# Kernel tuning notes

Hardware: AMD Instinct MI355X
Metric: run time of the kernel (lower is better)

## Reference

```python
import jax, jax.numpy as jnp
import numpy as np

N = 8192          # nodes per type (MiRNA, Disease, T)
E = 500000        # edges per relation
FEAT = 256
HID = 64
OUT = 128
ITEM = 8192
SIZE = 4096
LEFT = 0
# relation order: 0:MvsD(M->D) 1:DvsM(D->M) 2:MvsT(M->T) 3:TvsM(T->M) 4:TvsD(T->D) 5:DvsT(D->T)


def graph_conv(x, W, b, src, dst, n_src, n_dst):
    outdeg = jax.ops.segment_sum(jnp.ones(src.shape, x.dtype), src, num_segments=n_src)
    xs = (x * (jnp.maximum(outdeg, 1.0) ** -0.5)[:, None]) @ W
    agg = jax.ops.segment_sum(xs[src], dst, num_segments=n_dst)
    indeg = jax.ops.segment_sum(jnp.ones(dst.shape, x.dtype), dst, num_segments=n_dst)
    return agg * (jnp.maximum(indeg, 1.0) ** -0.5)[:, None] + b


def hetero_layer(hM, hD, hT, W, b, edges):
    srcs = [hM, hD, hM, hT, hT, hD]
    outs = [graph_conv(srcs[i], W[i], b[i], edges[i, 0], edges[i, 1], N, N) for i in range(6)]
    # aggregate='sum' per destination type
    newM = outs[1] + outs[3]
    newD = outs[0] + outs[4]
    newT = outs[2] + outs[5]
    return newM, newD, newT


def setup_inputs() -> dict:
    key = jax.random.key(0)
    ks = jax.random.split(key, 24)

    def glorot(k, shape):
        lim = np.sqrt(6.0 / (shape[-2] + shape[-1]))
        return jax.random.uniform(k, shape, jnp.float32, -lim, lim)

    inp = {
        'hM': jax.random.normal(ks[0], (N, FEAT), jnp.float32),
        'hD': jax.random.normal(ks[1], (N, FEAT), jnp.float32),
        'hT': jax.random.normal(ks[2], (N, FEAT), jnp.float32),
        'W1': glorot(ks[3], (6, FEAT, HID)), 'b1': jnp.zeros((6, HID), jnp.float32),
        'W2': glorot(ks[4], (6, HID, HID)), 'b2': jnp.zeros((6, HID), jnp.float32),
        'W3': glorot(ks[5], (6, HID, OUT)), 'b3': jnp.zeros((6, OUT), jnp.float32),
        'Adj': (jax.random.uniform(ks[6], (SIZE, ITEM)) < 0.05).astype(jnp.float32),
        'f1_w': glorot(ks[7], (ITEM + OUT, 256)), 'f1_b': jnp.zeros((256,), jnp.float32),
        'f2_w': glorot(ks[8], (256, 512)), 'f2_b': jnp.zeros((512,), jnp.float32),
        'f3_w': glorot(ks[9], (512, 1024)), 'f3_b': jnp.zeros((1024,), jnp.float32),
        'f4_w': glorot(ks[10], (1024, ITEM)), 'f4_b': jnp.zeros((ITEM,), jnp.float32),
        'edges': jax.random.randint(ks[11], (6, 2, E), 0, N, dtype=jnp.int32),
        'size': SIZE,
        'leftIndex': LEFT,
    }
    return inp


def reference(hM, hD, hT, W1, b1, W2, b2, W3, b3, Adj,
              f1_w, f1_b, f2_w, f2_b, f3_w, f3_b, f4_w, f4_b,
              edges, size, leftIndex):
    hM1, hD1, hT1 = hetero_layer(hM, hD, hT, W1, b1, edges)
    hM2, hD2, hT2 = hetero_layer(hM1, hD1, hT1, W2, b2, edges)
    hM3, hD3, hT3 = hetero_layer(hM2, hD2, hT2, W3, b3, edges)
    # torch.nn.functional.normalize(p=1, dim=1)
    mirna = hM3 / jnp.maximum(jnp.sum(jnp.abs(hM3), axis=1, keepdims=True), 1e-12)
    fake_embeding = mirna[leftIndex:leftIndex + size]
    M = jnp.concatenate([Adj, fake_embeding], axis=1)
    x = jax.nn.relu(M @ f1_w + f1_b)
    x = jax.nn.relu(x @ f2_w + f2_b)
    x = jax.nn.relu(x @ f3_w + f3_b)
    x = jax.nn.sigmoid(x @ f4_w + f4_b)
    return fake_embeding, x
```

## Files before the change

### kernel.cpp

```cpp
#include <hip/hip_runtime.h>
#include <hip/hip_bf16.h>
#include <cstdint>
#include <cstddef>
#include <type_traits>

#define NN 8192
#define NTYPE 6
#define BPT 32

typedef __attribute__((ext_vector_type(8))) short bf16x8;
typedef __attribute__((ext_vector_type(4))) float f32x4;
typedef __attribute__((ext_vector_type(4))) unsigned short u16x4;
typedef __attribute__((ext_vector_type(8))) unsigned short u16x8;

#define GLOAD16(g, l)                                                        \
  __builtin_amdgcn_global_load_lds(                                          \
      (const __attribute__((address_space(1))) void*)(g),                    \
      (__attribute__((address_space(3))) void*)(l), 16, 0, 0)

static __device__ __forceinline__ unsigned short f2bf(float f) {
  union { float f; unsigned u; } x; x.f = f;
  unsigned u = x.u + 0x7fffu + ((x.u >> 16) & 1u);
  return (unsigned short)(u >> 16);
}
static __device__ __forceinline__ float bf2f(unsigned short u) {
  union { unsigned u32; float f; } x; x.u32 = (unsigned)u << 16; return x.f;
}

__global__ __launch_bounds__(256) void hist_degree(
    const int* __restrict__ edges, int* __restrict__ partial, int E) {
  const int b = blockIdx.x, t = blockIdx.y, role = blockIdx.z;
  __shared__ int h[NN];
  for (int i = threadIdx.x; i < NN; i += 256) h[i] = 0;
  __syncthreads();
  const int* ids = edges + ((size_t)t * 2 + role) * E;
  int ch = (E + BPT - 1) / BPT;
  int beg = b * ch, end = (beg + ch < E) ? beg + ch : E;
  for (int i = beg + threadIdx.x; i < end; i += 256)
    atomicAdd(&h[__builtin_nontemporal_load(ids + i)], 1);
  __syncthreads();
  int* dst = partial + ((size_t)((role * NTYPE + t) * BPT + b)) * NN;
  for (int i = threadIdx.x; i < NN; i += 256) dst[i] = h[i];
}

__global__ __launch_bounds__(256) void reduce_deg(
    const int* __restrict__ partial, float* __restrict__ inv_out,
    float* __restrict__ inv_in, int* __restrict__ incnt) {
  int i = blockIdx.x * 256 + threadIdx.x;
  if (i >= NTYPE * NN) return;
  int t = i >> 13, n = i & (NN - 1);
  const int* ps = partial + ((size_t)(t * BPT)) * NN + n;
  const int* pd = partial + ((size_t)((NTYPE + t) * BPT)) * NN + n;
  int so = 0, sd = 0;
#pragma unroll 8
  for (int b = 0; b < BPT; ++b) { so += ps[(size_t)b * NN]; sd += pd[(size_t)b * NN]; }
  inv_out[i] = rsqrtf(fmaxf((float)so, 1.0f));
  inv_in[i]  = rsqrtf(fmaxf((float)sd, 1.0f));
  incnt[i]   = sd;
}

__global__ void scan_rows(const int* __restrict__ incnt, int* __restrict__ row_start) {
  int t = blockIdx.x;
  int i = threadIdx.x;
  const int* c = incnt + t * NN;
  int v[8], s = 0;
#pragma unroll
  for (int j = 0; j < 8; ++j) { v[j] = c[i * 8 + j]; s += v[j]; }
  __shared__ int p[1024];
  p[i] = s;
  __syncthreads();
  for (int d = 1; d < 1024; d <<= 1) {
    int x = (i >= d) ? p[i - d] : 0;
    __syncthreads();
    p[i] += x;
    __syncthreads();
  }
  int run = p[i] - s;
  int* rs = row_start + t * (NN + 1);
#pragma unroll
  for (int j = 0; j < 8; ++j) { rs[i * 8 + j] = run; run += v[j]; }
  if (i == 1023) rs[NN] = run;
}

__global__ __launch_bounds__(256) void slice_offsets(
    const int* __restrict__ partial, const int* __restrict__ row_start,
    int* __restrict__ soff) {
  int i = blockIdx.x * 256 + threadIdx.x;
  if (i >= NTYPE * NN) return;
  int t = i >> 13, d = i & (NN - 1);
  const int* pd = partial + ((size_t)((NTYPE + t) * BPT)) * NN + d;
  int run = row_start[t * (NN + 1) + d];
  int* o = soff + ((size_t)t * BPT) * NN + d;
#pragma unroll 8
  for (int s = 0; s < BPT; ++s) { o[(size_t)s * NN] = run; run += pd[(size_t)s * NN]; }
}

__global__ __launch_bounds__(256) void scatter_v2(
    const int* __restrict__ edges, const int* __restrict__ soff,
    int* __restrict__ csr, int E) {
  int t = blockIdx.x;
  if (t >= NTYPE) return;
  int s = blockIdx.y;
  __shared__ int cur[NN];
  const int* o = soff + ((size_t)(t * BPT + s)) * NN;
  for (int i = threadIdx.x; i < NN; i += 256) cur[i] = o[i];
  __syncthreads();
  int ch = (E + BPT - 1) / BPT;
  int beg = s * ch, end = (beg + ch < E) ? beg + ch : E;
  const int* eb = edges + (size_t)t * 2 * E;
  int* out = csr + (size_t)t * E;
  for (int i = beg + threadIdx.x; i < end; i += 256) {
    int src = __builtin_nontemporal_load(eb + i);
    int dst = __builtin_nontemporal_load(eb + E + i);
    int pos = atomicAdd(&cur[dst], 1);
    out[pos] = src;
  }
}

__global__ __launch_bounds__(256) void gemm64xs(
    const float* __restrict__ p0, const float* __restrict__ p1,
    const float* __restrict__ p2, int lda,
    const float* __restrict__ WL, const float* __restrict__ inv_out,
    unsigned short* __restrict__ xs6, int F, int H, int tpack) {
  const int t = (tpack >> (4 * blockIdx.z)) & 15;
  const int srcc[6] = {0, 1, 0, 2, 2, 1};
  const float* A = (srcc[t] == 0) ? p0 : (srcc[t] == 1) ? p1 : p2;
  const float* B = WL + (size_t)t * F * H;
  const float* rscale = inv_out + t * NN;
  unsigned short* out = xs6 + (size_t)t * NN * H;

  __shared__ float As[16][68];
  __shared__ float Bs[16][68];
  int tid = threadIdx.x;
  int n0 = blockIdx.x * 64, m0 = blockIdx.y * 64;
  int ar = tid >> 2, ac = (tid & 3) * 4;
  int br = tid >> 4, bc = (tid & 15) * 4;
  int tx = tid & 15, ty = tid >> 4;
  float acc[4][4] = {};
  for (int k0 = 0; k0 < F; k0 += 16) {
    float4 av = *(const float4*)(A + (size_t)(m0 + ar) * lda + k0 + ac);
    As[ac + 0][ar] = av.x; As[ac + 1][ar] = av.y;
    As[ac + 2][ar] = av.z; As[ac + 3][ar] = av.w;
    *(float4*)&Bs[br][bc] = *(const float4*)(B + (size_t)(k0 + br) * H + n0 + bc);
    __syncthreads();
#pragma unroll
    for (int kk = 0; kk < 16; ++kk) {
      float4 a = *(const float4*)&As[kk][ty * 4];
      float4 b = *(const float4*)&Bs[kk][tx * 4];
      float aa[4] = {a.x, a.y, a.z, a.w};
      float bb[4] = {b.x, b.y, b.z, b.w};
#pragma unroll
      for (int i = 0; i < 4; ++i)
#pragma unroll
        for (int j = 0; j < 4; ++j) acc[i][j] += aa[i] * bb[j];
    }
    __syncthreads();
  }
#pragma unroll
  for (int i = 0; i < 4; ++i) {
    int r = m0 + ty * 4 + i;
    float sc = rscale[r];
    union { unsigned short us[4]; short4 v; } pk;
#pragma unroll
    for (int j = 0; j < 4; ++j) pk.us[j] = f2bf(acc[i][j] * sc);
    *(short4*)&out[(size_t)r * H + n0 + tx * 4] = pk.v;
  }
}

template <int H>
__global__ __launch_bounds__(256) void aggregate3(
    const unsigned short* __restrict__ xs6, const int* __restrict__ csr,
    const int* __restrict__ row_start, const float* __restrict__ inv_in,
    const float* __restrict__ bL, float* __restrict__ feat_out, int E, int cpack) {
  constexpr int VE = H / 16;
  const int c = (cpack >> (8 * blockIdx.y)) & 0xff;
  const int taT[3] = {1, 0, 2}, tbT[3] = {3, 4, 5};
  int wave = threadIdx.x >> 6, lane = threadIdx.x & 63;
  int slot = lane >> 4, colg = lane & 15;
  int d = blockIdx.x * 4 + wave;

  float out[VE];
#pragma unroll
  for (int v = 0; v < VE; ++v) out[v] = 0.f;

#pragma unroll
  for (int half = 0; half < 2; ++half) {
    int t = half ? tbT[c] : taT[c];
    const unsigned short* xs = xs6 + (size_t)t * NN * H;
    const int* cs = csr + (size_t)t * E;
    const int* rs = row_start + t * (NN + 1);
    int b = rs[d], e = rs[d + 1];
    float a[VE];
#pragma unroll
    for (int v = 0; v < VE; ++v) a[v] = 0.f;
    for (int j0 = b; j0 < e; j0 += 64) {
      int myj = j0 + lane;
      int idxv = (myj < e) ? cs[myj] : 0;
      int cnt = e - j0; if (cnt > 64) cnt = 64;
      int g = 0;
      for (; (g + 1) * 4 <= cnt; ++g) {
        int is = __shfl(idxv, g * 4 + slot);
        const unsigned short* xr = xs + (size_t)is * H + colg * VE;
        if constexpr (VE == 4) {
          u16x4 x = *(const u16x4*)xr;
#pragma unroll
          for (int v = 0; v < 4; ++v) a[v] += bf2f(x[v]);
        } else {
          u16x8 x = *(const u16x8*)xr;
#pragma unroll
          for (int v = 0; v < 8; ++v) a[v] += bf2f(x[v]);
        }
      }
      int done = g * 4;
      if (done < cnt) {
        int gi = done + slot;
        int is = __shfl(idxv, gi < cnt ? gi : 0);
        float wt = (gi < cnt) ? 1.0f : 0.0f;
        const unsigned short* xr = xs + (size_t)is * H + colg * VE;
        if constexpr (VE == 4) {
          u16x4 x = *(const u16x4*)xr;
#pragma unroll
          for (int v = 0; v < 4; ++v) a[v] += wt * bf2f(x[v]);
        } else {
          u16x8 x = *(const u16x8*)xr;
#pragma unroll
          for (int v = 0; v < 8; ++v) a[v] += wt * bf2f(x[v]);
        }
      }
    }
    float sc = inv_in[t * NN + d];
#pragma unroll
    for (int v = 0; v < VE; ++v) out[v] += a[v] * sc;
  }
#pragma unroll
  for (int v = 0; v < VE; ++v) {
    out[v] += __shfl_xor(out[v], 16);
    out[v] += __shfl_xor(out[v], 32);
  }
  if (lane < 16) {
    int ta = taT[c], tb = tbT[c];
    float* o = feat_out + (size_t)c * NN * 128 + (size_t)d * H + colg * VE;
    const float* ba = bL + ta * H + colg * VE;
    const float* bb = bL + tb * H + colg * VE;
    float4 w0 = make_float4(out[0] + ba[0] + bb[0], out[1] + ba[1] + bb[1],
                            out[2] + ba[2] + bb[2], out[3] + ba[3] + bb[3]);
    *(float4*)o = w0;
    if constexpr (VE == 8) {
      float4 w1 = make_float4(out[4] + ba[4] + bb[4], out[5] + ba[5] + bb[5],
                              out[6] + ba[6] + bb[6], out[7] + ba[7] + bb[7]);
      *(float4*)(o + 4) = w1;
    }
  }
}

__global__ __launch_bounds__(256) void l1norm_fake(
    const float* __restrict__ hM3, const int* __restrict__ leftIndex,
    float* __restrict__ fake) {
  int wave = threadIdx.x >> 6, lane = threadIdx.x & 63;
  int r = blockIdx.x * 4 + wave;
  int row = leftIndex[0] + r;
  const float* x = hM3 + (size_t)row * 128;
  float a = x[lane], b = x[64 + lane];
  float s = fabsf(a) + fabsf(b);
#pragma unroll
  for (int d = 1; d < 64; d <<= 1) s += __shfl_xor(s, d);
  float inv = 1.0f / fmaxf(s, 1e-12f);
  fake[(size_t)r * 128 + lane]      = a * inv;
  fake[(size_t)r * 128 + 64 + lane] = b * inv;
}

__global__ __launch_bounds__(256) void castT(
    const float* __restrict__ in, unsigned short* __restrict__ out, int K, int N) {
  __shared__ float t[32][33];
  int k0 = blockIdx.y * 32, n0 = blockIdx.x * 32;
  int tx = threadIdx.x & 31, ty = threadIdx.x >> 5;
#pragma unroll
  for (int i = 0; i < 32; i += 8)
    t[ty + i][tx] = in[(size_t)(k0 + ty + i) * N + n0 + tx];
  __syncthreads();
#pragma unroll
  for (int i = 0; i < 32; i += 8)
    out[(size_t)(n0 + ty + i) * K + k0 + tx] = f2bf(t[tx][ty + i]);
}

template <int ASRC, int ACT>
__global__ __launch_bounds__(256) void mfma_gemm(
    const unsigned short* __restrict__ Abf, int lda,
    const float* __restrict__ A1, const float* __restrict__ A2,
    int K1, int lda1, int lda2,
    const unsigned short* __restrict__ Bt, int ldb,
    const float* __restrict__ bias,
    void* __restrict__ outp, int ldo, int K, int kchunk, int pstride) {
  __shared__ unsigned short As[128 * 32];
  __shared__ unsigned short Bs[128 * 32];
  const int tid = threadIdx.x;
  const int n0 = blockIdx.x * 128, m0 = blockIdx.y * 128;
  const int wave = tid >> 6, lane = tid & 63;
  const int lq = lane >> 4, lr = lane & 15;
  const int wm = wave >> 1, wn = wave & 1;
  const int kbeg = blockIdx.z * kchunk;
  const int kend = (kbeg + kchunk < K) ? (kbeg + kchunk) : K;

  f32x4 acc[4][4] = {};

  const int G0 = tid, G1 = tid + 256;
  const int r0 = G0 >> 2, c0 = ((G0 & 3) - (r0 >> 1)) & 3;
  const int r1 = G1 >> 2, c1 = ((G1 & 3) - (r1 >> 1)) & 3;
  const int wbase0 = (tid & ~63) * 8;
  const int wbase1 = wbase0 + 256 * 8;

  for (int k0 = kbeg; k0 < kend; k0 += 32) {
    GLOAD16(Bt + (size_t)(n0 + r0) * ldb + k0 + c0 * 8, &Bs[wbase0]);
    GLOAD16(Bt + (size_t)(n0 + r1) * ldb + k0 + c1 * 8, &Bs[wbase1]);
    if (ASRC == 0) {
      GLOAD16(Abf + (size_t)(m0 + r0) * lda + k0 + c0 * 8, &As[wbase0]);
      GLOAD16(Abf + (size_t)(m0 + r1) * lda + k0 + c1 * 8, &As[wbase1]);
    } else {
#pragma unroll
      for (int q = 0; q < 2; ++q) {
        int r = q ? r1 : r0, c = q ? c1 : c0, G = q ? G1 : G0;
        int kk = k0 + c * 8;
        const float* src = (kk < K1) ? (A1 + (size_t)(m0 + r) * lda1 + kk)
                                     : (A2 + (size_t)(m0 + r) * lda2 + (kk - K1));
        float4 u = *(const float4*)src;
        float4 v = *(const float4*)(src + 4);
        union { unsigned short us[8]; bf16x8 v8; } pk;
        pk.us[0] = f2bf(u.x); pk.us[1] = f2bf(u.y);
        pk.us[2] = f2bf(u.z); pk.us[3] = f2bf(u.w);
        pk.us[4] = f2bf(v.x); pk.us[5] = f2bf(v.y);
        pk.us[6] = f2bf(v.z); pk.us[7] = f2bf(v.w);
        *(bf16x8*)&As[G * 8] = pk.v8;
      }
    }
    __syncthreads();

    const int cs = (lq + (lr >> 1)) & 3;
    const int rA = wm * 64 + lr, rB = wn * 64 + lr;
    bf16x8 af[4], bfr[4];
#pragma unroll
    for (int m = 0; m < 4; ++m)
      af[m] = *(const bf16x8*)&As[(((rA + m * 16) << 2) + cs) << 3];
#pragma unroll
    for (int n = 0; n < 4; ++n)
      bfr[n] = *(const bf16x8*)&Bs[(((rB + n * 16) << 2) + cs) << 3];
#pragma unroll
    for (int m = 0; m < 4; ++m)
#pragma unroll
      for (int n = 0; n < 4; ++n)
        acc[m][n] = __builtin_amdgcn_mfma_f32_16x16x32_bf16(af[m], bfr[n], acc[m][n], 0, 0, 0);
    __syncthreads();
  }

  const int rowb = m0 + wm * 64 + lq * 4;
  const int colb = n0 + wn * 64 + lr;
  float* pout = (ACT == 0) ? ((float*)outp + (size_t)blockIdx.z * pstride) : (float*)outp;
#pragma unroll
  for (int n = 0; n < 4; ++n) {
    int c = colb + n * 16;
    float bv = (ACT == 0) ? 0.0f : bias[c];
#pragma unroll
    for (int m = 0; m < 4; ++m) {
      int r = rowb + m * 16;
#pragma unroll
      for (int j = 0; j < 4; ++j) {
        float v = acc[m][n][j] + bv;
        if (ACT == 0) {
          pout[(size_t)(r + j) * ldo + c] = v;
        } else {
          v = fmaxf(v, 0.0f);
          ((unsigned short*)outp)[(size_t)(r + j) * ldo + c] = f2bf(v);
        }
      }
    }
  }
}

__global__ __launch_bounds__(512, 2) void gemm256sig(
    const unsigned short* __restrict__ A, int lda,
    const unsigned short* __restrict__ Bt, int ldb,
    const float* __restrict__ bias,
    float* __restrict__ out, int ldo) {
  __shared__ unsigned short A0[8192], A1[8192], A2[8192], A3[8192];
  __shared__ unsigned short B0[8192], B1[8192], B2[8192], B3[8192];
  const int tid = threadIdx.x;
  const int wave = tid >> 6, lane = tid & 63;
  const int lq = lane >> 4, lr = lane & 15;
  const int wm = wave >> 2, wn = wave & 3;
  const int bid = blockIdx.x;
  const int xcd = bid & 7, kb = bid >> 3;
  const int n0 = (xcd * 4 + (kb & 3)) * 256;
  const int m0 = (kb >> 2) * 256;

  f32x4 acc[8][4] = {};

  const int G0 = tid, G1 = tid + 512;
  const int ra0 = G0 >> 2, ca0 = ((G0 & 3) - (ra0 >> 1)) & 3;
  const int ra1 = G1 >> 2, ca1 = ((G1 & 3) - (ra1 >> 1)) & 3;
  const int d0 = wave * 512, d1 = d0 + 4096;

  auto issue = [&](unsigned short* na, unsigned short* nb, int h) {
    int kk = h * 32;
    GLOAD16(A  + (size_t)(m0 + ra0) * lda + kk + ca0 * 8, na + d0);
    GLOAD16(A  + (size_t)(m0 + ra1) * lda + kk + ca1 * 8, na + d1);
    GLOAD16(Bt + (size_t)(n0 + ra0) * ldb + kk + ca0 * 8, nb + d0);
    GLOAD16(Bt + (size_t)(n0 + ra1) * ldb + kk + ca1 * 8, nb + d1);
  };

  auto step = [&](auto WC, const unsigned short* sa, const unsigned short* sb,
                  unsigned short* na, unsigned short* nb, int hnext) {
    asm volatile("s_waitcnt vmcnt(%0)" :: "i"(decltype(WC)::value) : "memory");
    __builtin_amdgcn_s_barrier();
    __builtin_amdgcn_sched_barrier(0);
    bf16x8 afv[8], bfv[4];
#pragma unroll
    for (int n = 0; n < 4; ++n) {
      int r = wn * 64 + n * 16 + lr;
      bfv[n] = *(const bf16x8*)&sb[(size_t)(((r << 2) + ((lq + (r >> 1)) & 3)) << 3)];
    }
#pragma unroll
    for (int m = 0; m < 4; ++m) {
      int r = wm * 128 + m * 16 + lr;
      afv[m] = *(const bf16x8*)&sa[(size_t)(((r << 2) + ((lq + (r >> 1)) & 3)) << 3)];
    }
    if (hnext >= 0) issue(na, nb, hnext);
    __builtin_amdgcn_s_setprio(1);
#pragma unroll
    for (int m = 0; m < 4; ++m)
#pragma unroll
      for (int n = 0; n < 4; ++n)
        acc[m][n] = __builtin_amdgcn_mfma_f32_16x16x32_bf16(afv[m], bfv[n], acc[m][n], 0, 0, 0);
    __builtin_amdgcn_s_setprio(0);
#pragma unroll
    for (int m = 4; m < 8; ++m) {
      int r = wm * 128 + m * 16 + lr;
      afv[m] = *(const bf16x8*)&sa[(size_t)(((r << 2) + ((lq + (r >> 1)) & 3)) << 3)];
    }
    __builtin_amdgcn_s_setprio(1);
#pragma unroll
    for (int m = 4; m < 8; ++m)
#pragma unroll
      for (int n = 0; n < 4; ++n)
        acc[m][n] = __builtin_amdgcn_mfma_f32_16x16x32_bf16(afv[m], bfv[n], acc[m][n], 0, 0, 0);
    __builtin_amdgcn_s_setprio(0);
  };

  using ic8 = std::integral_constant<int, 8>;
  using ic4 = std::integral_constant<int, 4>;
  using ic0 = std::integral_constant<int, 0>;

  issue(A0, B0, 0); issue(A1, B1, 1); issue(A2, B2, 2);

#pragma unroll 1
  for (int t = 0; t < 7; ++t) {
    int h = t * 4;
    step(ic8{}, A0, B0, A3, B3, h + 3);
    step(ic8{}, A1, B1, A0, B0, h + 4);
    step(ic8{}, A2, B2, A1, B1, h + 5);
    step(ic8{}, A3, B3, A2, B2, h + 6);
  }
  step(ic8{}, A0, B0, A3, B3, 31);
  step(ic8{}, A1, B1, nullptr, nullptr, -1);
  step(ic4{}, A2, B2, nullptr, nullptr, -1);
  step(ic0{}, A3, B3, nullptr, nullptr, -1);

  __builtin_amdgcn_s_barrier();
  float* lw;
  switch (wave) {
    case 0: lw = (float*)A0; break;
    case 1: lw = (float*)A1; break;
    case 2: lw = (float*)A2; break;
    case 3: lw = (float*)A3; break;
    case 4: lw = (float*)B0; break;
    case 5: lw = (float*)B1; break;
    case 6: lw = (float*)B2; break;
    default: lw = (float*)B3; break;
  }
  const int rowb = m0 + wm * 128;
  const int colb = n0 + wn * 64;
  float bv[4];
#pragma unroll
  for (int n = 0; n < 4; ++n) bv[n] = bias[colb + n * 16 + lr];
#pragma unroll
  for (int m = 0; m < 8; ++m) {
#pragma unroll
    for (int n = 0; n < 4; ++n)
#pragma unroll
      for (int j = 0; j < 4; ++j) {
        float v = acc[m][n][j] + bv[n];
        v = 1.0f / (1.0f + __expf(-v));
        lw[(lq * 4 + j) * 68 + n * 16 + lr] = v;
      }
    asm volatile("s_waitcnt lgkmcnt(0)" ::: "memory");
#pragma unroll
    for (int i = 0; i < 4; ++i) {
      int chunk = i * 64 + lane;
      int rr = chunk >> 4, cg = chunk & 15;
      f32x4 val = *(f32x4*)&lw[rr * 68 + cg * 4];
      __builtin_nontemporal_store(
          val, (f32x4*)(out + (size_t)(rowb + m * 16 + rr) * ldo + colb + cg * 4));
    }
    asm volatile("s_waitcnt lgkmcnt(0)" ::: "memory");
  }
}

__global__ __launch_bounds__(256) void reduceK(
    const float* __restrict__ part, const float* __restrict__ bias,
    unsigned short* __restrict__ out, int total, int N, int nsplit, int pstride) {
  int idx = blockIdx.x * 256 + threadIdx.x;
  int base = idx * 4;
  if (base >= total) return;
  float4 s = *(const float4*)(part + base);
  for (int z = 1; z < nsplit; ++z) {
    float4 p = *(const float4*)(part + (size_t)z * pstride + base);
    s.x += p.x; s.y += p.y; s.z += p.z; s.w += p.w;
  }
  float4 bv = *(const float4*)(bias + (base & (N - 1)));
  union { unsigned short us[4]; short4 v; } pk;
  pk.us[0] = f2bf(fmaxf(s.x + bv.x, 0.0f));
  pk.us[1] = f2bf(fmaxf(s.y + bv.y, 0.0f));
  pk.us[2] = f2bf(fmaxf(s.z + bv.z, 0.0f));
  pk.us[3] = f2bf(fmaxf(s.w + bv.w, 0.0f));
  *(short4*)&out[base] = pk.v;
}

extern "C" void kernel_launch(void* const* d_in, const int* in_sizes, int n_in,
                              void* d_out, int out_size, void* d_ws, size_t ws_size,
                              hipStream_t stream) {
  const float* hM  = (const float*)d_in[0];
  const float* hD  = (const float*)d_in[1];
  const float* hT  = (const float*)d_in[2];
  const float* W1  = (const float*)d_in[3];
  const float* b1  = (const float*)d_in[4];
  const float* W2  = (const float*)d_in[5];
  const float* b2  = (const float*)d_in[6];
  const float* W3  = (const float*)d_in[7];
  const float* b3  = (const float*)d_in[8];
  const float* Adj = (const float*)d_in[9];
  const float* f1w = (const float*)d_in[10];
  const float* f1b = (const float*)d_in[11];
  const float* f2w = (const float*)d_in[12];
  const float* f2b = (const float*)d_in[13];
  const float* f3w = (const float*)d_in[14];
  const float* f3b = (const float*)d_in[15];
  const float* f4w = (const float*)d_in[16];
  const float* f4b = (const float*)d_in[17];
  const int* edges = (const int*)d_in[18];
  const int* leftIndex = (const int*)d_in[20];
  const int E = in_sizes[18] / 12;
  (void)ws_size; (void)n_in; (void)out_size;

  char* w = (char*)d_ws;
  size_t off = 0;
  auto alloc = [&](size_t bytes) {
    void* p = w + off;
    off = (off + bytes + 255) & ~(size_t)255;
    return p;
  };
  int*   row_start = (int*)  alloc((size_t)NTYPE * (NN + 1) * 4);
  int*   incnt     = (int*)  alloc((size_t)NTYPE * NN * 4);
  float* inv_out   = (float*)alloc((size_t)NTYPE * NN * 4);
  float* inv_in    = (float*)alloc((size_t)NTYPE * NN * 4);
  float* featA     = (float*)alloc((size_t)3 * NN * 128 * 4);
  size_t ubase = off;
  int*            csr   = (int*)           alloc((size_t)NTYPE * E * 4);
  unsigned short* xs6   = (unsigned short*)alloc((size_t)NTYPE * NN * 128 * 2);
  float*          featB = (float*)         alloc((size_t)3 * NN * 128 * 4);
  int* deg_part = (int*)csr;
  int* soff     = (int*)featB;
  size_t moff = ubase;
  auto malloc2 = [&](size_t bytes) {
    void* p = w + moff;
    moff = (moff + bytes + 255) & ~(size_t)255;
    return p;
  };
  unsigned short* w1t = (unsigned short*)malloc2((size_t)256 * 8320 * 2);
  unsigned short* w2t = (unsigned short*)malloc2((size_t)512 * 256 * 2);
  unsigned short* w3t = (unsigned short*)malloc2((size_t)1024 * 512 * 2);
  unsigned short* w4t = (unsigned short*)malloc2((size_t)8192 * 1024 * 2);
  unsigned short* x1b = (unsigned short*)malloc2((size_t)4096 * 256 * 2);
  unsigned short* x2b = (unsigned short*)malloc2((size_t)4096 * 512 * 2);
  unsigned short* x3b = (unsigned short*)malloc2((size_t)4096 * 1024 * 2);
  float*          x1p = (float*)malloc2((size_t)4 * 4096 * 256 * 4);

  hist_degree<<<dim3(BPT, NTYPE, 2), 256, 0, stream>>>(edges, deg_part, E);
  reduce_deg<<<(NTYPE * NN + 255) / 256, 256, 0, stream>>>(deg_part, inv_out, inv_in, incnt);
  scan_rows<<<NTYPE, 1024, 0, stream>>>(incnt, row_start);
  slice_offsets<<<(NTYPE * NN + 255) / 256, 256, 0, stream>>>(deg_part, row_start, soff);
  scatter_v2<<<dim3(8, BPT), 256, 0, stream>>>(edges, soff, csr, E);

  const size_t comp = (size_t)NN * 128;
  gemm64xs<<<dim3(1, NN / 64, 6), 256, 0, stream>>>(
      hM, hD, hT, 256, W1, inv_out, xs6, 256, 64, 0x543210);
  aggregate3<64><<<dim3(NN / 4, 3), 256, 0, stream>>>(
      xs6, csr, row_start, inv_in, b1, featA, E, 0x020100);
  gemm64xs<<<dim3(1, NN / 64, 4), 256, 0, stream>>>(
      featA, featA + comp, featA + 2 * comp, 64, W2, inv_out, xs6, 64, 64, 0x5420);
  aggregate3<64><<<dim3(NN / 4, 2), 256, 0, stream>>>(
      xs6, csr, row_start, inv_in, b2, featB, E, 0x0201);
  gemm64xs<<<dim3(2, NN / 64, 2), 256, 0, stream>>>(
      featB, featB + comp, featB + 2 * comp, 64, W3, inv_out, xs6, 64, 128, 0x31);
  aggregate3<128><<<dim3(NN / 4, 1), 256, 0, stream>>>(
      xs6, csr, row_start, inv_in, b3, featA, E, 0x00);

  float* fake = (float*)d_out;
  float* outx = (float*)d_out + (size_t)4096 * 128;
  l1norm_fake<<<4096 / 4, 256, 0, stream>>>(featA, leftIndex, fake);

  castT<<<dim3(256 / 32, 8320 / 32), 256, 0, stream>>>(f1w, w1t, 8320, 256);
  castT<<<dim3(512 / 32, 256 / 32), 256, 0, stream>>>(f2w, w2t, 256, 512);
  castT<<<dim3(1024 / 32, 512 / 32), 256, 0, stream>>>(f3w, w3t, 512, 1024);
  castT<<<dim3(8192 / 32, 1024 / 32), 256, 0, stream>>>(f4w, w4t, 1024, 8192);

  mfma_gemm<1, 0><<<dim3(256 / 128, 4096 / 128, 4), 256, 0, stream>>>(
      nullptr, 0, Adj, fake, 8192, 8192, 128, w1t, 8320, nullptr,
      x1p, 256, 8320, 2080, 4096 * 256);
  reduceK<<<(4096 * 256 / 4 + 255) / 256, 256, 0, stream>>>(
      x1p, f1b, x1b, 4096 * 256, 256, 4, 4096 * 256);
  mfma_gemm<0, 1><<<dim3(512 / 128, 4096 / 128), 256, 0, stream>>>(
      x1b, 256, nullptr, nullptr, 0, 0, 0, w2t, 256, f2b, x2b, 512, 256, 256, 0);
  mfma_gemm<0, 1><<<dim3(1024 / 128, 4096 / 128), 256, 0, stream>>>(
      x2b, 512, nullptr, nullptr, 0, 0, 0, w3t, 512, f3b, x3b, 1024, 512, 512, 0);
  gemm256sig<<<512, 512, 0, stream>>>(x3b, 1024, w4t, 1024, f4b, outx, 8192);
}
```

Measured before the change: 435.2 us.

## Replace 4-stage direct-to-LDS pipeline with register-staged double buffering in sigmoid GEMM

The final sigmoid GEMM previously streamed tiles straight into a 4-deep ring of LDS buffers using global_load_lds, with vmcnt-based waits. It now loads each K-slice into registers, writes them to one of two LDS buffers, and keeps one slice of global loads in flight, with a __syncthreads per iteration. This halves LDS use and changes launch bounds to one block per SM. The trade is extra register pressure and VGPR-to-LDS write instructions, shallower prefetch depth, and lower occupancy, which may expose more global-memory latency.

```diff
diff --git a/kernel.cpp b/kernel.cpp
--- a/kernel.cpp
+++ b/kernel.cpp
@@ -375,13 +375,13 @@
   }
 }
 
-__global__ __launch_bounds__(512, 2) void gemm256sig(
+__global__ __launch_bounds__(512, 1) void gemm256sig(
     const unsigned short* __restrict__ A, int lda,
     const unsigned short* __restrict__ Bt, int ldb,
     const float* __restrict__ bias,
     float* __restrict__ out, int ldo) {
-  __shared__ unsigned short A0[8192], A1[8192], A2[8192], A3[8192];
-  __shared__ unsigned short B0[8192], B1[8192], B2[8192], B3[8192];
+  __shared__ unsigned short sA[2][8192];
+  __shared__ unsigned short sB[2][8192];
   const int tid = threadIdx.x;
   const int wave = tid >> 6, lane = tid & 63;
   const int lq = lane >> 4, lr = lane & 15;
@@ -393,88 +393,61 @@
 
   f32x4 acc[8][4] = {};
 
-  const int G0 = tid, G1 = tid + 512;
-  const int ra0 = G0 >> 2, ca0 = ((G0 & 3) - (ra0 >> 1)) & 3;
-  const int ra1 = G1 >> 2, ca1 = ((G1 & 3) - (ra1 >> 1)) & 3;
-  const int d0 = wave * 512, d1 = d0 + 4096;
-
-  auto issue = [&](unsigned short* na, unsigned short* nb, int h) {
+  const int ra0 = tid >> 2, ca0 = tid & 3;
+  const int ra1 = ra0 + 128, ca1 = ca0;
+  const int sl0 = (ra0 << 2) + ((ca0 + (ra0 >> 1)) & 3);
+  const int sl1 = (ra1 << 2) + ((ca1 + (ra1 >> 1)) & 3);
+
+  u16x8 gA0, gA1, gB0, gB1;
+  auto g_issue = [&](int h) {
     int kk = h * 32;
-    GLOAD16(A  + (size_t)(m0 + ra0) * lda + kk + ca0 * 8, na + d0);
-    GLOAD16(A  + (size_t)(m0 + ra1) * lda + kk + ca1 * 8, na + d1);
-    GLOAD16(Bt + (size_t)(n0 + ra0) * ldb + kk + ca0 * 8, nb + d0);
-    GLOAD16(Bt + (size_t)(n0 + ra1) * ldb + kk + ca1 * 8, nb + d1);
+    gA0 = *(const u16x8*)(A  + (size_t)(m0 + ra0) * lda + kk + ca0 * 8);
+    gA1 = *(const u16x8*)(A  + (size_t)(m0 + ra1) * lda + kk + ca1 * 8);
+    gB0 = *(const u16x8*)(Bt + (size_t)(n0 + ra0) * ldb + kk + ca0 * 8);
+    gB1 = *(const u16x8*)(Bt + (size_t)(n0 + ra1) * ldb + kk + ca1 * 8);
   };
-
-  auto step = [&](auto WC, const unsigned short* sa, const unsigned short* sb,
-                  unsigned short* na, unsigned short* nb, int hnext) {
-    asm volatile("s_waitcnt vmcnt(%0)" :: "i"(decltype(WC)::value) : "memory");
-    __builtin_amdgcn_s_barrier();
-    __builtin_amdgcn_sched_barrier(0);
+  auto l_write = [&](int buf) {
+    *(u16x8*)&sA[buf][sl0 * 8] = gA0;
+    *(u16x8*)&sA[buf][sl1 * 8] = gA1;
+    *(u16x8*)&sB[buf][sl0 * 8] = gB0;
+    *(u16x8*)&sB[buf][sl1 * 8] = gB1;
+  };
+
+  g_issue(0);
+  l_write(0);
+  g_issue(1);
+  __syncthreads();
+
+#pragma unroll 1
+  for (int h = 0; h < 32; ++h) {
+    const int cur = h & 1, nxt = cur ^ 1;
+    const unsigned short* pa = &sA[cur][0];
+    const unsigned short* pb = &sB[cur][0];
     bf16x8 afv[8], bfv[4];
 #pragma unroll
     for (int n = 0; n < 4; ++n) {
       int r = wn * 64 + n * 16 + lr;
-      bfv[n] = *(const bf16x8*)&sb[(size_t)(((r << 2) + ((lq + (r >> 1)) & 3)) << 3)];
-    }
-#pragma unroll
-    for (int m = 0; m < 4; ++m) {
+      bfv[n] = *(const bf16x8*)&pb[(size_t)(((r << 2) + ((lq + (r >> 1)) & 3)) << 3)];
+    }
+#pragma unroll
+    for (int m = 0; m < 8; ++m) {
       int r = wm * 128 + m * 16 + lr;
-      afv[m] = *(const bf16x8*)&sa[(size_t)(((r << 2) + ((lq + (r >> 1)) & 3)) << 3)];
-    }
-    if (hnext >= 0) issue(na, nb, hnext);
+      afv[m] = *(const bf16x8*)&pa[(size_t)(((r << 2) + ((lq + (r >> 1)) & 3)) << 3)];
+    }
+    if (h + 1 < 32) l_write(nxt);
+    if (h + 2 < 32) g_issue(h + 2);
     __builtin_amdgcn_s_setprio(1);
 #pragma unroll
-    for (int m = 0; m < 4; ++m)
+    for (int m = 0; m < 8; ++m)
 #pragma unroll
       for (int n = 0; n < 4; ++n)
         acc[m][n] = __builtin_amdgcn_mfma_f32_16x16x32_bf16(afv[m], bfv[n], acc[m][n], 0, 0, 0);
     __builtin_amdgcn_s_setprio(0);
-#pragma unroll
-    for (int m = 4; m < 8; ++m) {
-      int r = wm * 128 + m * 16 + lr;
-      afv[m] = *(const bf16x8*)&sa[(size_t)(((r << 2) + ((lq + (r >> 1)) & 3)) << 3)];
-    }
-    __builtin_amdgcn_s_setprio(1);
-#pragma unroll
-    for (int m = 4; m < 8; ++m)
-#pragma unroll
-      for (int n = 0; n < 4; ++n)
-        acc[m][n] = __builtin_amdgcn_mfma_f32_16x16x32_bf16(afv[m], bfv[n], acc[m][n], 0, 0, 0);
-    __builtin_amdgcn_s_setprio(0);
-  };
-
-  using ic8 = std::integral_constant<int, 8>;
-  using ic4 = std::integral_constant<int, 4>;
-  using ic0 = std::integral_constant<int, 0>;
-
-  issue(A0, B0, 0); issue(A1, B1, 1); issue(A2, B2, 2);
-
-#pragma unroll 1
-  for (int t = 0; t < 7; ++t) {
-    int h = t * 4;
-    step(ic8{}, A0, B0, A3, B3, h + 3);
-    step(ic8{}, A1, B1, A0, B0, h + 4);
-    step(ic8{}, A2, B2, A1, B1, h + 5);
-    step(ic8{}, A3, B3, A2, B2, h + 6);
-  }
-  step(ic8{}, A0, B0, A3, B3, 31);
-  step(ic8{}, A1, B1, nullptr, nullptr, -1);
-  step(ic4{}, A2, B2, nullptr, nullptr, -1);
-  step(ic0{}, A3, B3, nullptr, nullptr, -1);
-
-  __builtin_amdgcn_s_barrier();
-  float* lw;
-  switch (wave) {
-    case 0: lw = (float*)A0; break;
-    case 1: lw = (float*)A1; break;
-    case 2: lw = (float*)A2; break;
-    case 3: lw = (float*)A3; break;
-    case 4: lw = (float*)B0; break;
-    case 5: lw = (float*)B1; break;
-    case 6: lw = (float*)B2; break;
-    default: lw = (float*)B3; break;
-  }
+    __syncthreads();
+  }
+
+  float* lw = (wave < 4) ? ((float*)&sA[0][0] + wave * 2048)
+                         : ((float*)&sB[0][0] + (wave - 4) * 2048);
   const int rowb = m0 + wm * 128;
   const int colb = n0 + wn * 64;
   float bv[4];
```

Result: no change. 433.8 us (-0.3%).
